# Performance work log

Measured on AMD Instinct MI355X. Metric: run time of the kernel, lower is better.

## Reference

```python
import jax, jax.numpy as jnp
import numpy as np

B, T, D = 4, 2048, 512
E, H, K = 8, 512, 2


def setup_inputs() -> dict:
    key = jax.random.key(0)
    ks = jax.random.split(key, 8)
    s_in = 1.0 / np.sqrt(D)
    s_h = 1.0 / np.sqrt(H)
    return {
        "x": jax.random.normal(ks[0], (B, T, D), dtype=jnp.float32),
        "Wg": jax.random.uniform(ks[1], (D, E), jnp.float32, -s_in, s_in),
        "bg": jax.random.uniform(ks[2], (E,), jnp.float32, -s_in, s_in),
        "W1": jax.random.uniform(ks[3], (E, D, H), jnp.float32, -s_in, s_in),
        "b1": jax.random.uniform(ks[4], (E, H), jnp.float32, -s_in, s_in),
        "W2": jax.random.uniform(ks[5], (E, H, H), jnp.float32, -s_h, s_h),
        "b2": jax.random.uniform(ks[6], (E, H), jnp.float32, -s_h, s_h),
    }


def reference(x, Wg, bg, W1, b1, W2, b2):
    Bx, Tx, Dx = x.shape
    xf = x.reshape(-1, Dx)                                   # [N, D]
    # --- gate (noise_std = 0) ---
    logits = xf @ Wg + bg                                    # [N, E]
    topk_scores, topk_idx = jax.lax.top_k(logits, K)         # [N, K]
    topk_w = jax.nn.softmax(topk_scores, axis=-1)            # K=2 -> softmax over selected
    # --- experts: dense compute, then gather the selected ones ---
    h = jax.nn.gelu(jnp.einsum('nd,edh->neh', xf, W1) + b1, approximate=False)  # [N, E, H]
    y = jnp.einsum('neh,ehf->nef', h, W2) + b2               # [N, E, H]
    sel = jnp.take_along_axis(y, topk_idx[:, :, None], axis=1)  # [N, K, H]
    out = jnp.sum(topk_w[:, :, None] * sel, axis=1)          # weighted combine [N, H]
    return out.reshape(Bx, Tx, -1)
```

## Files before the change

### kernel.cpp

```cpp
#include <hip/hip_runtime.h>
#include <hip/hip_bf16.h>


typedef __bf16 bf16x8 __attribute__((ext_vector_type(8)));
typedef float  f32x4  __attribute__((ext_vector_type(4)));

#define N_TOK 8192
#define D_IN  512
#define N_EXP 8
#define H_DIM 512
#define TILE  32

static __device__ __forceinline__ unsigned short f2bf(float f) {
    union { float f; unsigned u; } v; v.f = f;
    unsigned r = v.u + 0x7FFFu + ((v.u >> 16) & 1u);
    return (unsigned short)(r >> 16);
}
static __device__ __forceinline__ float bf2f(unsigned short h) {
    union { unsigned u; float f; } v; v.u = ((unsigned)h) << 16; return v.f;
}

__global__ void __launch_bounds__(256) k_pack(const float* __restrict__ W1,
                                              const float* __restrict__ W2,
                                              unsigned short* __restrict__ w1f,
                                              unsigned short* __restrict__ w2f) {
    __shared__ float t[32][65];
    int z = blockIdx.z;
    int e = z & 7;
    const float* in = (z < 8) ? W1 : W2;
    unsigned short* out = (z < 8) ? w1f : w2f;
    int cb0 = blockIdx.x * 4;
    int kc  = blockIdx.y;
    const float* src = in + ((size_t)e * 512 + kc * 32) * 512 + blockIdx.x * 64;
    int tid = threadIdx.x;
    int r = tid >> 3, cq = (tid & 7) * 8;
    float4 v0 = *(const float4*)(src + (size_t)r * 512 + cq);
    float4 v1 = *(const float4*)(src + (size_t)r * 512 + cq + 4);
    t[r][cq + 0] = v0.x; t[r][cq + 1] = v0.y; t[r][cq + 2] = v0.z; t[r][cq + 3] = v0.w;
    t[r][cq + 4] = v1.x; t[r][cq + 5] = v1.y; t[r][cq + 6] = v1.z; t[r][cq + 7] = v1.w;
    __syncthreads();
    int g = tid >> 6, lane = tid & 63;
    int l15 = lane & 15, l4 = lane >> 4;
    unsigned v[4];
    #pragma unroll
    for (int j = 0; j < 4; ++j) {
        unsigned lo = f2bf(t[l4 * 8 + 2 * j    ][g * 16 + l15]);
        unsigned hi = f2bf(t[l4 * 8 + 2 * j + 1][g * 16 + l15]);
        v[j] = lo | (hi << 16);
    }
    size_t dst = (((size_t)(e * 32 + cb0 + g) * 16 + kc) * 512) + lane * 8;
    *(uint4*)(out + dst) = make_uint4(v[0], v[1], v[2], v[3]);
}

__global__ void __launch_bounds__(256) k_gate(const float* __restrict__ x,
                                              const float* __restrict__ Wg,
                                              const float* __restrict__ bg,
                                              unsigned char* __restrict__ sel,
                                              float2* __restrict__ w2,
                                              unsigned short* __restrict__ xbf) {
    __shared__ float part[32][8][8];
    __shared__ float lg[32][8];
    int tid = threadIdx.x;
    int t = tid >> 3, c = tid & 7;
    int n0 = blockIdx.x * 32;
    int n = n0 + t;
    const float4* xr = (const float4*)(x + (size_t)n * D_IN + c * 64);
    float acc[8];
    #pragma unroll
    for (int e = 0; e < 8; ++e) acc[e] = 0.f;
    #pragma unroll
    for (int j4 = 0; j4 < 16; ++j4) {
        float4 v = xr[j4];
        int k = c * 64 + j4 * 4;
        float xv[4] = {v.x, v.y, v.z, v.w};
        #pragma unroll
        for (int u = 0; u < 4; ++u) {
            float4 wlo = *(const float4*)(Wg + (size_t)(k + u) * 8);
            float4 whi = *(const float4*)(Wg + (size_t)(k + u) * 8 + 4);
            acc[0] += xv[u] * wlo.x; acc[1] += xv[u] * wlo.y;
            acc[2] += xv[u] * wlo.z; acc[3] += xv[u] * wlo.w;
            acc[4] += xv[u] * whi.x; acc[5] += xv[u] * whi.y;
            acc[6] += xv[u] * whi.z; acc[7] += xv[u] * whi.w;
        }
    }
    #pragma unroll
    for (int e = 0; e < 8; ++e) part[t][c][e] = acc[e];
    __syncthreads();
    {
        float f = bg[c];
        #pragma unroll
        for (int cc = 0; cc < 8; ++cc) f += part[t][cc][c];
        lg[t][c] = f;
    }
    __syncthreads();
    if (c == 0) {
        float best = lg[t][0]; int i1 = 0;
        #pragma unroll
        for (int j = 1; j < 8; ++j) { float v = lg[t][j]; if (v > best) { best = v; i1 = j; } }
        float best2 = -1e30f; int i2 = 0;
        #pragma unroll
        for (int j = 0; j < 8; ++j) {
            if (j == i1) continue;
            float v = lg[t][j]; if (v > best2) { best2 = v; i2 = j; }
        }
        float tt = expf(best2 - best);
        float w0 = 1.0f / (1.0f + tt);
        sel[n] = (unsigned char)(i1 | (i2 << 4));
        w2[n] = make_float2(w0, 1.0f - w0);
    }
    #pragma unroll
    for (int i = 0; i < 8; ++i) {
        int idx = tid + i * 256;
        int r = idx >> 6, g = idx & 63;
        const float* src = x + (size_t)(n0 + r) * D_IN + g * 8;
        float4 a = *(const float4*)src;
        float4 b = *(const float4*)(src + 4);
        unsigned u0 = (unsigned)f2bf(a.x) | ((unsigned)f2bf(a.y) << 16);
        unsigned u1 = (unsigned)f2bf(a.z) | ((unsigned)f2bf(a.w) << 16);
        unsigned u2 = (unsigned)f2bf(b.x) | ((unsigned)f2bf(b.y) << 16);
        unsigned u3 = (unsigned)f2bf(b.z) | ((unsigned)f2bf(b.w) << 16);
        *(uint4*)(xbf + (size_t)(n0 + r) * D_IN + g * 8) = make_uint4(u0, u1, u2, u3);
    }
}

__global__ void __launch_bounds__(1024) k_build(const unsigned char* __restrict__ sel,
                                                const float2* __restrict__ w2,
                                                int* __restrict__ counts,
                                                int* __restrict__ lists,
                                                float* __restrict__ wgts) {
    int e = blockIdx.x;
    __shared__ int wave_tot[16], wave_base[16];
    int tid = threadIdx.x;
    int lane = tid & 63, wv = tid >> 6;
    int base = 0;
    for (int c0 = 0; c0 < N_TOK; c0 += 1024) {
        int n = c0 + tid;
        unsigned char s = sel[n];
        bool f1 = ((s & 15) == e);
        bool f = f1 || ((s >> 4) == e);
        unsigned long long mask = __ballot(f);
        int prefix = __popcll(mask & ((1ull << lane) - 1ull));
        if (lane == 0) wave_tot[wv] = __popcll(mask);
        __syncthreads();
        if (tid < 16) {
            int wb = 0;
            for (int i = 0; i < tid; ++i) wb += wave_tot[i];
            wave_base[tid] = wb;
        }
        __syncthreads();
        if (f) {
            int pos = base + wave_base[wv] + prefix;
            lists[e * N_TOK + pos] = (n << 1) | (f1 ? 0 : 1);
            float2 w = w2[n];
            wgts[e * N_TOK + pos] = f1 ? w.x : w.y;
        }
        base += wave_base[15] + wave_tot[15];
        __syncthreads();
    }
    if (tid == 0) counts[e] = base;
}

template <bool SLOT>
__global__ void __launch_bounds__(512, 4)
k_experts(const unsigned short* __restrict__ xbf,
          const unsigned short* __restrict__ w1f, const float* __restrict__ b1,
          const unsigned short* __restrict__ w2f, const float* __restrict__ b2,
          const int* __restrict__ counts, const int* __restrict__ lists,
          const float* __restrict__ wgts,
          unsigned short* __restrict__ ybuf, float* __restrict__ out) {
    __shared__ unsigned short lds[TILE * D_IN];
    __shared__ int   tl[TILE];
    __shared__ float wl[TILE];

    int b = blockIdx.x;
    int e = b & 7;
    int tile = b >> 3;
    int cnt = counts[e];
    int row0 = tile * TILE;
    if (row0 >= cnt) return;
    int rv = min(TILE, cnt - row0);

    int tid = threadIdx.x;
    int lane = tid & 63;
    int wid = tid >> 6;
    int cw = wid * 64;
    int l15 = lane & 15, l4 = lane >> 4;

    if (tid < TILE) {
        int v = 0; float w = 0.f;
        if (tid < rv) {
            v = lists[e * N_TOK + row0 + tid];
            w = wgts [e * N_TOK + row0 + tid];
        }
        tl[tid] = v; wl[tid] = w;
    }
    __syncthreads();

    #pragma unroll
    for (int it = 0; it < 4; ++it) {
        int idx = tid + it * 512;
        int r = idx >> 6, g = idx & 63;
        uint4 v = make_uint4(0, 0, 0, 0);
        if (r < rv)
            v = *(const uint4*)(xbf + (size_t)(tl[r] >> 1) * D_IN + g * 8);
        int off = (r * 1024 + g * 16) ^ ((r & 7) << 4);
        *(uint4*)((char*)lds + off) = v;
    }
    __syncthreads();

    const unsigned short* w1base = w1f + ((size_t)(e * 32 + wid * 4) * 16) * 512 + (size_t)lane * 8;
    f32x4 acc[2][4];
    #pragma unroll
    for (int n = 0; n < 4; ++n) {
        float bv = b1[e * H_DIM + cw + n * 16 + l15];
        #pragma unroll
        for (int m = 0; m < 2; ++m) acc[m][n] = f32x4{bv, bv, bv, bv};
    }
    {
        bf16x8 bb[4][4];
        #pragma unroll
        for (int n = 0; n < 4; ++n) {
            bb[0][n] = *(const bf16x8*)(w1base + (n * 16 + 0) * 512);
            bb[1][n] = *(const bf16x8*)(w1base + (n * 16 + 1) * 512);
            bb[2][n] = *(const bf16x8*)(w1base + (n * 16 + 2) * 512);
        }
        #pragma unroll
        for (int kc = 0; kc < 16; ++kc) {
            if (kc + 3 < 16) {
                #pragma unroll
                for (int n = 0; n < 4; ++n)
                    bb[(kc + 3) & 3][n] = *(const bf16x8*)(w1base + (n * 16 + kc + 3) * 512);
            }
            int k0 = kc * 32 + l4 * 8;
            bf16x8 a[2];
            #pragma unroll
            for (int m = 0; m < 2; ++m) {
                int row = m * 16 + l15;
                int off = (row * 1024 + k0 * 2) ^ ((row & 7) << 4);
                a[m] = *(const bf16x8*)((const char*)lds + off);
            }
            #pragma unroll
            for (int n = 0; n < 4; ++n)
                #pragma unroll
                for (int m = 0; m < 2; ++m)
                    acc[m][n] = __builtin_amdgcn_mfma_f32_16x16x32_bf16(a[m], bb[kc & 3][n], acc[m][n], 0, 0, 0);
        }
    }
    __syncthreads();

    #pragma unroll
    for (int m = 0; m < 2; ++m)
        #pragma unroll
        for (int n = 0; n < 4; ++n)
            #pragma unroll
            for (int r = 0; r < 4; ++r) {
                int row = m * 16 + l4 * 4 + r;
                int col = cw + n * 16 + l15;
                float v = acc[m][n][r];
                float g = 0.5f * v * (1.0f + erff(v * 0.70710678118654752f));
                int off = (row * 1024 + col * 2) ^ ((row & 7) << 4);
                *(unsigned short*)((char*)lds + off) = f2bf(g);
            }
    __syncthreads();

    const unsigned short* w2base = w2f + ((size_t)(e * 32 + wid * 4) * 16) * 512 + (size_t)lane * 8;
    #pragma unroll
    for (int n = 0; n < 4; ++n) {
        float bv = b2[e * H_DIM + cw + n * 16 + l15];
        #pragma unroll
        for (int m = 0; m < 2; ++m) acc[m][n] = f32x4{bv, bv, bv, bv};
    }
    {
        bf16x8 bb[4][4];
        #pragma unroll
        for (int n = 0; n < 4; ++n) {
            bb[0][n] = *(const bf16x8*)(w2base + (n * 16 + 0) * 512);
            bb[1][n] = *(const bf16x8*)(w2base + (n * 16 + 1) * 512);
            bb[2][n] = *(const bf16x8*)(w2base + (n * 16 + 2) * 512);
        }
        #pragma unroll
        for (int kc = 0; kc < 16; ++kc) {
            if (kc + 3 < 16) {
                #pragma unroll
                for (int n = 0; n < 4; ++n)
                    bb[(kc + 3) & 3][n] = *(const bf16x8*)(w2base + (n * 16 + kc + 3) * 512);
            }
            int k0 = kc * 32 + l4 * 8;
            bf16x8 a[2];
            #pragma unroll
            for (int m = 0; m < 2; ++m) {
                int row = m * 16 + l15;
                int off = (row * 1024 + k0 * 2) ^ ((row & 7) << 4);
                a[m] = *(const bf16x8*)((const char*)lds + off);
            }
            #pragma unroll
            for (int n = 0; n < 4; ++n)
                #pragma unroll
                for (int m = 0; m < 2; ++m)
                    acc[m][n] = __builtin_amdgcn_mfma_f32_16x16x32_bf16(a[m], bb[kc & 3][n], acc[m][n], 0, 0, 0);
        }
    }

    if (SLOT) {
        __syncthreads();
        #pragma unroll
        for (int m = 0; m < 2; ++m)
            #pragma unroll
            for (int n = 0; n < 4; ++n)
                #pragma unroll
                for (int r = 0; r < 4; ++r) {
                    int row = m * 16 + l4 * 4 + r;
                    int col = cw + n * 16 + l15;
                    lds[row * 512 + col] = f2bf(acc[m][n][r] * wl[row]);
                }
        __syncthreads();
        #pragma unroll
        for (int rr = 0; rr < 4; ++rr) {
            int row = wid * 4 + rr;
            if (row < rv) {
                int v = tl[row];
                uint4 d = *(uint4*)((char*)lds + row * 1024 + lane * 16);
                *(uint4*)(ybuf + (size_t)v * H_DIM + lane * 8) = d;
            }
        }
    } else {
        #pragma unroll
        for (int m = 0; m < 2; ++m)
            #pragma unroll
            for (int r = 0; r < 4; ++r) {
                int row = m * 16 + l4 * 4 + r;
                if (row < rv) {
                    int t = tl[row] >> 1;
                    float gw = wl[row];
                    #pragma unroll
                    for (int n = 0; n < 4; ++n) {
                        int col = cw + n * 16 + l15;
                        atomicAdd(out + (size_t)t * H_DIM + col, gw * acc[m][n][r]);
                    }
                }
            }
    }
}

__global__ void __launch_bounds__(256) k_combine(const unsigned short* __restrict__ yb,
                                                 float* __restrict__ out) {
    int gid = blockIdx.x * 256 + threadIdx.x;
    int n = gid >> 6;
    int h0 = (gid & 63) * 8;
    const unsigned short* r0 = yb + ((size_t)2 * n) * H_DIM + h0;
    uint4 a = *(const uint4*)r0;
    uint4 b = *(const uint4*)(r0 + H_DIM);
    float o[8];
    unsigned ua[4] = {a.x, a.y, a.z, a.w}, ub[4] = {b.x, b.y, b.z, b.w};
    #pragma unroll
    for (int j = 0; j < 4; ++j) {
        o[2 * j]     = bf2f((unsigned short)(ua[j] & 0xFFFF)) + bf2f((unsigned short)(ub[j] & 0xFFFF));
        o[2 * j + 1] = bf2f((unsigned short)(ua[j] >> 16))    + bf2f((unsigned short)(ub[j] >> 16));
    }
    float* dst = out + (size_t)n * H_DIM + h0;
    *(float4*)dst       = make_float4(o[0], o[1], o[2], o[3]);
    *(float4*)(dst + 4) = make_float4(o[4], o[5], o[6], o[7]);
}

extern "C" void kernel_launch(void* const* d_in, const int* in_sizes, int n_in,
                              void* d_out, int out_size, void* d_ws, size_t ws_size,
                              hipStream_t stream) {
    (void)in_sizes; (void)n_in;
    const float* x  = (const float*)d_in[0];
    const float* Wg = (const float*)d_in[1];
    const float* bg = (const float*)d_in[2];
    const float* W1 = (const float*)d_in[3];
    const float* b1 = (const float*)d_in[4];
    const float* W2 = (const float*)d_in[5];
    const float* b2 = (const float*)d_in[6];
    float* out = (float*)d_out;

    char* ws = (char*)d_ws;
    unsigned short* w1f = (unsigned short*)(ws);
    unsigned short* w2f = (unsigned short*)(ws + (4u << 20));
    unsigned short* ybuf= (unsigned short*)(ws + (8u << 20));
    unsigned short* xbf = (unsigned short*)(ws + (24u << 20));
    char* tail = ws + (32u << 20);
    int*   counts = (int*)(tail);
    int*   lists  = (int*)(tail + 256);
    float* wgts   = (float*)(tail + 256 + 262144);
    unsigned char* sel = (unsigned char*)(tail + 256 + 524288);
    float2* w2g   = (float2*)(tail + 256 + 532480);
    size_t need = (32u << 20) + 256 + 532480 + 65536;

    bool slot = ws_size >= need;
    if (!slot) {
        xbf  = (unsigned short*)(ws + (8u << 20));
        tail = ws + (16u << 20);
        counts = (int*)(tail);
        lists  = (int*)(tail + 256);
        wgts   = (float*)(tail + 256 + 262144);
        sel    = (unsigned char*)(tail + 256 + 524288);
        w2g    = (float2*)(tail + 256 + 532480);
        hipMemsetAsync(out, 0, (size_t)out_size * sizeof(float), stream);
    }

    k_pack<<<dim3(8, 16, 16), dim3(256), 0, stream>>>(W1, W2, w1f, w2f);
    k_gate<<<dim3(N_TOK / 32), dim3(256), 0, stream>>>(x, Wg, bg, sel, w2g, xbf);
    k_build<<<dim3(N_EXP), dim3(1024), 0, stream>>>(sel, w2g, counts, lists, wgts);
    if (slot) {
        k_experts<true><<<dim3(2048), dim3(512), 0, stream>>>(
            xbf, w1f, b1, w2f, b2, counts, lists, wgts, ybuf, out);
        k_combine<<<dim3(N_TOK * 64 / 256), dim3(256), 0, stream>>>(ybuf, out);
    } else {
        k_experts<false><<<dim3(2048), dim3(512), 0, stream>>>(
            xbf, w1f, b1, w2f, b2, counts, lists, wgts, ybuf, out);
    }
}
```

Before: 191.3 us.

## Double expert row tile to 64 and convert x to bf16 inside expert kernel

Each expert block now processes 64 gathered token rows as two 32-row halves that share every loaded weight fragment. This halves how often W1/W2 are reread from memory and halves the grid size. The separate bf16 copy of x written by the gate kernel is removed; the expert kernel gathers fp32 rows and converts them while staging into LDS. The cost is twice the accumulator registers and LDS per block, lower occupancy (launch bounds 512,2), and more wasted work on partially filled tiles.

```diff
diff --git a/kernel.cpp b/kernel.cpp
--- a/kernel.cpp
+++ b/kernel.cpp
@@ -9,7 +9,7 @@
 #define D_IN  512
 #define N_EXP 8
 #define H_DIM 512
-#define TILE  32
+#define TILE  64
 
 static __device__ __forceinline__ unsigned short f2bf(float f) {
     union { float f; unsigned u; } v; v.f = f;
@@ -56,14 +56,12 @@
                                               const float* __restrict__ Wg,
                                               const float* __restrict__ bg,
                                               unsigned char* __restrict__ sel,
-                                              float2* __restrict__ w2,
-                                              unsigned short* __restrict__ xbf) {
+                                              float2* __restrict__ w2) {
     __shared__ float part[32][8][8];
     __shared__ float lg[32][8];
     int tid = threadIdx.x;
     int t = tid >> 3, c = tid & 7;
-    int n0 = blockIdx.x * 32;
-    int n = n0 + t;
+    int n = blockIdx.x * 32 + t;
     const float4* xr = (const float4*)(x + (size_t)n * D_IN + c * 64);
     float acc[8];
     #pragma unroll
@@ -107,19 +105,6 @@
         float w0 = 1.0f / (1.0f + tt);
         sel[n] = (unsigned char)(i1 | (i2 << 4));
         w2[n] = make_float2(w0, 1.0f - w0);
-    }
-    #pragma unroll
-    for (int i = 0; i < 8; ++i) {
-        int idx = tid + i * 256;
-        int r = idx >> 6, g = idx & 63;
-        const float* src = x + (size_t)(n0 + r) * D_IN + g * 8;
-        float4 a = *(const float4*)src;
-        float4 b = *(const float4*)(src + 4);
-        unsigned u0 = (unsigned)f2bf(a.x) | ((unsigned)f2bf(a.y) << 16);
-        unsigned u1 = (unsigned)f2bf(a.z) | ((unsigned)f2bf(a.w) << 16);
-        unsigned u2 = (unsigned)f2bf(b.x) | ((unsigned)f2bf(b.y) << 16);
-        unsigned u3 = (unsigned)f2bf(b.z) | ((unsigned)f2bf(b.w) << 16);
-        *(uint4*)(xbf + (size_t)(n0 + r) * D_IN + g * 8) = make_uint4(u0, u1, u2, u3);
     }
 }
 
@@ -161,14 +146,15 @@
 }
 
 template <bool SLOT>
-__global__ void __launch_bounds__(512, 4)
-k_experts(const unsigned short* __restrict__ xbf,
+__global__ void __launch_bounds__(512, 2)
+k_experts(const float* __restrict__ x,
           const unsigned short* __restrict__ w1f, const float* __restrict__ b1,
           const unsigned short* __restrict__ w2f, const float* __restrict__ b2,
           const int* __restrict__ counts, const int* __restrict__ lists,
           const float* __restrict__ wgts,
           unsigned short* __restrict__ ybuf, float* __restrict__ out) {
-    __shared__ unsigned short lds[TILE * D_IN];
+    __shared__ unsigned short ldsA[32 * D_IN];
+    __shared__ unsigned short ldsB[32 * D_IN];
     __shared__ int   tl[TILE];
     __shared__ float wl[TILE];
 
@@ -197,53 +183,62 @@
     __syncthreads();
 
     #pragma unroll
-    for (int it = 0; it < 4; ++it) {
+    for (int it = 0; it < 16; ++it) {
         int idx = tid + it * 512;
-        int r = idx >> 6, g = idx & 63;
-        uint4 v = make_uint4(0, 0, 0, 0);
+        int r = idx >> 7, c4 = idx & 127;
+        float4 v = make_float4(0.f, 0.f, 0.f, 0.f);
         if (r < rv)
-            v = *(const uint4*)(xbf + (size_t)(tl[r] >> 1) * D_IN + g * 8);
-        int off = (r * 1024 + g * 16) ^ ((r & 7) << 4);
-        *(uint4*)((char*)lds + off) = v;
-    }
-    __syncthreads();
-
-    const unsigned short* w1base = w1f + ((size_t)(e * 32 + wid * 4) * 16) * 512 + (size_t)lane * 8;
-    f32x4 acc[2][4];
-    #pragma unroll
-    for (int n = 0; n < 4; ++n) {
-        float bv = b1[e * H_DIM + cw + n * 16 + l15];
-        #pragma unroll
-        for (int m = 0; m < 2; ++m) acc[m][n] = f32x4{bv, bv, bv, bv};
-    }
+            v = ((const float4*)(x + (size_t)(tl[r] >> 1) * D_IN))[c4];
+        unsigned lo = (unsigned)f2bf(v.x) | ((unsigned)f2bf(v.y) << 16);
+        unsigned hi = (unsigned)f2bf(v.z) | ((unsigned)f2bf(v.w) << 16);
+        int rr = r & 31;
+        int off = (rr * 1024 + c4 * 8) ^ ((rr & 7) << 4);
+        char* base = (r < 32) ? (char*)ldsA : (char*)ldsB;
+        *(uint2*)(base + off) = make_uint2(lo, hi);
+    }
+    __syncthreads();
+
+    f32x4 accA[2][4], accB[2][4];
+
     {
+        const unsigned short* wbase = w1f + ((size_t)(e * 32 + wid * 4) * 16) * 512 + (size_t)lane * 8;
+        #pragma unroll
+        for (int n = 0; n < 4; ++n) {
+            float bv = b1[e * H_DIM + cw + n * 16 + l15];
+            #pragma unroll
+            for (int m = 0; m < 2; ++m) { accA[m][n] = f32x4{bv, bv, bv, bv}; accB[m][n] = f32x4{bv, bv, bv, bv}; }
+        }
         bf16x8 bb[4][4];
         #pragma unroll
         for (int n = 0; n < 4; ++n) {
-            bb[0][n] = *(const bf16x8*)(w1base + (n * 16 + 0) * 512);
-            bb[1][n] = *(const bf16x8*)(w1base + (n * 16 + 1) * 512);
-            bb[2][n] = *(const bf16x8*)(w1base + (n * 16 + 2) * 512);
+            bb[0][n] = *(const bf16x8*)(wbase + (n * 16 + 0) * 512);
+            bb[1][n] = *(const bf16x8*)(wbase + (n * 16 + 1) * 512);
+            bb[2][n] = *(const bf16x8*)(wbase + (n * 16 + 2) * 512);
         }
         #pragma unroll
         for (int kc = 0; kc < 16; ++kc) {
             if (kc + 3 < 16) {
                 #pragma unroll
                 for (int n = 0; n < 4; ++n)
-                    bb[(kc + 3) & 3][n] = *(const bf16x8*)(w1base + (n * 16 + kc + 3) * 512);
+                    bb[(kc + 3) & 3][n] = *(const bf16x8*)(wbase + (n * 16 + kc + 3) * 512);
             }
             int k0 = kc * 32 + l4 * 8;
-            bf16x8 a[2];
+            bf16x8 aA[2], aB[2];
             #pragma unroll
             for (int m = 0; m < 2; ++m) {
                 int row = m * 16 + l15;
                 int off = (row * 1024 + k0 * 2) ^ ((row & 7) << 4);
-                a[m] = *(const bf16x8*)((const char*)lds + off);
-            }
-            #pragma unroll
-            for (int n = 0; n < 4; ++n)
-                #pragma unroll
-                for (int m = 0; m < 2; ++m)
-                    acc[m][n] = __builtin_amdgcn_mfma_f32_16x16x32_bf16(a[m], bb[kc & 3][n], acc[m][n], 0, 0, 0);
+                aA[m] = *(const bf16x8*)((const char*)ldsA + off);
+                aB[m] = *(const bf16x8*)((const char*)ldsB + off);
+            }
+            #pragma unroll
+            for (int n = 0; n < 4; ++n) {
+                #pragma unroll
+                for (int m = 0; m < 2; ++m) {
+                    accA[m][n] = __builtin_amdgcn_mfma_f32_16x16x32_bf16(aA[m], bb[kc & 3][n], accA[m][n], 0, 0, 0);
+                    accB[m][n] = __builtin_amdgcn_mfma_f32_16x16x32_bf16(aB[m], bb[kc & 3][n], accB[m][n], 0, 0, 0);
+                }
+            }
         }
     }
     __syncthreads();
@@ -256,48 +251,55 @@
             for (int r = 0; r < 4; ++r) {
                 int row = m * 16 + l4 * 4 + r;
                 int col = cw + n * 16 + l15;
-                float v = acc[m][n][r];
-                float g = 0.5f * v * (1.0f + erff(v * 0.70710678118654752f));
                 int off = (row * 1024 + col * 2) ^ ((row & 7) << 4);
-                *(unsigned short*)((char*)lds + off) = f2bf(g);
-            }
-    __syncthreads();
-
-    const unsigned short* w2base = w2f + ((size_t)(e * 32 + wid * 4) * 16) * 512 + (size_t)lane * 8;
-    #pragma unroll
-    for (int n = 0; n < 4; ++n) {
-        float bv = b2[e * H_DIM + cw + n * 16 + l15];
-        #pragma unroll
-        for (int m = 0; m < 2; ++m) acc[m][n] = f32x4{bv, bv, bv, bv};
-    }
+                float vA = accA[m][n][r];
+                float gA = 0.5f * vA * (1.0f + erff(vA * 0.70710678118654752f));
+                *(unsigned short*)((char*)ldsA + off) = f2bf(gA);
+                float vB = accB[m][n][r];
+                float gB = 0.5f * vB * (1.0f + erff(vB * 0.70710678118654752f));
+                *(unsigned short*)((char*)ldsB + off) = f2bf(gB);
+            }
+    __syncthreads();
+
     {
+        const unsigned short* wbase = w2f + ((size_t)(e * 32 + wid * 4) * 16) * 512 + (size_t)lane * 8;
+        #pragma unroll
+        for (int n = 0; n < 4; ++n) {
+            float bv = b2[e * H_DIM + cw + n * 16 + l15];
+            #pragma unroll
+            for (int m = 0; m < 2; ++m) { accA[m][n] = f32x4{bv, bv, bv, bv}; accB[m][n] = f32x4{bv, bv, bv, bv}; }
+        }
         bf16x8 bb[4][4];
         #pragma unroll
         for (int n = 0; n < 4; ++n) {
-            bb[0][n] = *(const bf16x8*)(w2base + (n * 16 + 0) * 512);
-            bb[1][n] = *(const bf16x8*)(w2base + (n * 16 + 1) * 512);
-            bb[2][n] = *(const bf16x8*)(w2base + (n * 16 + 2) * 512);
+            bb[0][n] = *(const bf16x8*)(wbase + (n * 16 + 0) * 512);
+            bb[1][n] = *(const bf16x8*)(wbase + (n * 16 + 1) * 512);
+            bb[2][n] = *(const bf16x8*)(wbase + (n * 16 + 2) * 512);
         }
         #pragma unroll
         for (int kc = 0; kc < 16; ++kc) {
             if (kc + 3 < 16) {
                 #pragma unroll
                 for (int n = 0; n < 4; ++n)
-                    bb[(kc + 3) & 3][n] = *(const bf16x8*)(w2base + (n * 16 + kc + 3) * 512);
+                    bb[(kc + 3) & 3][n] = *(const bf16x8*)(wbase + (n * 16 + kc + 3) * 512);
             }
             int k0 = kc * 32 + l4 * 8;
-            bf16x8 a[2];
+            bf16x8 aA[2], aB[2];
             #pragma unroll
             for (int m = 0; m < 2; ++m) {
                 int row = m * 16 + l15;
                 int off = (row * 1024 + k0 * 2) ^ ((row & 7) << 4);
-                a[m] = *(const bf16x8*)((const char*)lds + off);
-            }
-            #pragma unroll
-            for (int n = 0; n < 4; ++n)
-                #pragma unroll
-                for (int m = 0; m < 2; ++m)
-                    acc[m][n] = __builtin_amdgcn_mfma_f32_16x16x32_bf16(a[m], bb[kc & 3][n], acc[m][n], 0, 0, 0);
+                aA[m] = *(const bf16x8*)((const char*)ldsA + off);
+                aB[m] = *(const bf16x8*)((const char*)ldsB + off);
+            }
+            #pragma unroll
+            for (int n = 0; n < 4; ++n) {
+                #pragma unroll
+                for (int m = 0; m < 2; ++m) {
+                    accA[m][n] = __builtin_amdgcn_mfma_f32_16x16x32_bf16(aA[m], bb[kc & 3][n], accA[m][n], 0, 0, 0);
+                    accB[m][n] = __builtin_amdgcn_mfma_f32_16x16x32_bf16(aB[m], bb[kc & 3][n], accB[m][n], 0, 0, 0);
+                }
+            }
         }
     }
 
@@ -311,15 +313,17 @@
                 for (int r = 0; r < 4; ++r) {
                     int row = m * 16 + l4 * 4 + r;
                     int col = cw + n * 16 + l15;
-                    lds[row * 512 + col] = f2bf(acc[m][n][r] * wl[row]);
+                    ldsA[row * 512 + col] = f2bf(accA[m][n][r] * wl[row]);
+                    ldsB[row * 512 + col] = f2bf(accB[m][n][r] * wl[row + 32]);
                 }
         __syncthreads();
         #pragma unroll
-        for (int rr = 0; rr < 4; ++rr) {
-            int row = wid * 4 + rr;
+        for (int rr = 0; rr < 8; ++rr) {
+            int row = wid * 8 + rr;
             if (row < rv) {
                 int v = tl[row];
-                uint4 d = *(uint4*)((char*)lds + row * 1024 + lane * 16);
+                const unsigned short* src = (row < 32) ? ldsA : ldsB;
+                uint4 d = *(uint4*)((char*)src + (row & 31) * 1024 + lane * 16);
                 *(uint4*)(ybuf + (size_t)v * H_DIM + lane * 8) = d;
             }
         }
@@ -328,15 +332,15 @@
         for (int m = 0; m < 2; ++m)
             #pragma unroll
             for (int r = 0; r < 4; ++r) {
-                int row = m * 16 + l4 * 4 + r;
-                if (row < rv) {
-                    int t = tl[row] >> 1;
-                    float gw = wl[row];
-                    #pragma unroll
-                    for (int n = 0; n < 4; ++n) {
-                        int col = cw + n * 16 + l15;
-                        atomicAdd(out + (size_t)t * H_DIM + col, gw * acc[m][n][r]);
-                    }
+                int rowA = m * 16 + l4 * 4 + r;
+                int rowB = rowA + 32;
+                #pragma unroll
+                for (int n = 0; n < 4; ++n) {
+                    int col = cw + n * 16 + l15;
+                    if (rowA < rv)
+                        atomicAdd(out + (size_t)(tl[rowA] >> 1) * H_DIM + col, wl[rowA] * accA[m][n][r]);
+                    if (rowB < rv)
+                        atomicAdd(out + (size_t)(tl[rowB] >> 1) * H_DIM + col, wl[rowB] * accB[m][n][r]);
                 }
             }
     }
@@ -379,19 +383,17 @@
     unsigned short* w1f = (unsigned short*)(ws);
     unsigned short* w2f = (unsigned short*)(ws + (4u << 20));
     unsigned short* ybuf= (unsigned short*)(ws + (8u << 20));
-    unsigned short* xbf = (unsigned short*)(ws + (24u << 20));
-    char* tail = ws + (32u << 20);
+    char* tail = ws + (24u << 20);
     int*   counts = (int*)(tail);
     int*   lists  = (int*)(tail + 256);
     float* wgts   = (float*)(tail + 256 + 262144);
     unsigned char* sel = (unsigned char*)(tail + 256 + 524288);
     float2* w2g   = (float2*)(tail + 256 + 532480);
-    size_t need = (32u << 20) + 256 + 532480 + 65536;
+    size_t need = (24u << 20) + 256 + 532480 + 65536;
 
     bool slot = ws_size >= need;
     if (!slot) {
-        xbf  = (unsigned short*)(ws + (8u << 20));
-        tail = ws + (16u << 20);
+        tail = ws + (8u << 20);
         counts = (int*)(tail);
         lists  = (int*)(tail + 256);
         wgts   = (float*)(tail + 256 + 262144);
@@ -401,14 +403,14 @@
     }
 
     k_pack<<<dim3(8, 16, 16), dim3(256), 0, stream>>>(W1, W2, w1f, w2f);
-    k_gate<<<dim3(N_TOK / 32), dim3(256), 0, stream>>>(x, Wg, bg, sel, w2g, xbf);
+    k_gate<<<dim3(N_TOK / 32), dim3(256), 0, stream>>>(x, Wg, bg, sel, w2g);
     k_build<<<dim3(N_EXP), dim3(1024), 0, stream>>>(sel, w2g, counts, lists, wgts);
     if (slot) {
-        k_experts<true><<<dim3(2048), dim3(512), 0, stream>>>(
-            xbf, w1f, b1, w2f, b2, counts, lists, wgts, ybuf, out);
+        k_experts<true><<<dim3(1024), dim3(512), 0, stream>>>(
+            x, w1f, b1, w2f, b2, counts, lists, wgts, ybuf, out);
         k_combine<<<dim3(N_TOK * 64 / 256), dim3(256), 0, stream>>>(ybuf, out);
     } else {
-        k_experts<false><<<dim3(2048), dim3(512), 0, stream>>>(
-            xbf, w1f, b1, w2f, b2, counts, lists, wgts, ybuf, out);
-    }
-}
+        k_experts<false><<<dim3(1024), dim3(512), 0, stream>>>(
+            x, w1f, b1, w2f, b2, counts, lists, wgts, ybuf, out);
+    }
+}
```

Result: no change. 188.1 us (-1.7%).

## Split fused expert MLP into separate layer kernels with 64-row tiles

Applied to the files above, without the earlier changes.

The single fused expert kernel (32-row tiles, both layers in one block) becomes two kernels. k_l1 gathers fp32 x rows, converts them to bf16 in LDS, and writes GELU(h) as bf16 to a padded global buffer. k_l2 reads that buffer and applies the second layer. Each block now handles 64 rows and half of the output columns, so every weight fragment is reused across more rows, and the x-to-bf16 conversion in the gate kernel is removed. The cost is an extra global write and read of the hidden activations, an additional launch, and 64KB of LDS per block, which may limit occupancy.

```diff
diff --git a/kernel.cpp b/kernel.cpp
--- a/kernel.cpp
+++ b/kernel.cpp
@@ -9,7 +9,6 @@
 #define D_IN  512
 #define N_EXP 8
 #define H_DIM 512
-#define TILE  32
 
 static __device__ __forceinline__ unsigned short f2bf(float f) {
     union { float f; unsigned u; } v; v.f = f;
@@ -18,6 +17,9 @@
 }
 static __device__ __forceinline__ float bf2f(unsigned short h) {
     union { unsigned u; float f; } v; v.u = ((unsigned)h) << 16; return v.f;
+}
+static __device__ __forceinline__ float gelu_exact(float v) {
+    return 0.5f * v * (1.0f + erff(v * 0.70710678118654752f));
 }
 
 __global__ void __launch_bounds__(256) k_pack(const float* __restrict__ W1,
@@ -56,14 +58,12 @@
                                               const float* __restrict__ Wg,
                                               const float* __restrict__ bg,
                                               unsigned char* __restrict__ sel,
-                                              float2* __restrict__ w2,
-                                              unsigned short* __restrict__ xbf) {
+                                              float2* __restrict__ w2) {
     __shared__ float part[32][8][8];
     __shared__ float lg[32][8];
     int tid = threadIdx.x;
     int t = tid >> 3, c = tid & 7;
-    int n0 = blockIdx.x * 32;
-    int n = n0 + t;
+    int n = blockIdx.x * 32 + t;
     const float4* xr = (const float4*)(x + (size_t)n * D_IN + c * 64);
     float acc[8];
     #pragma unroll
@@ -107,19 +107,6 @@
         float w0 = 1.0f / (1.0f + tt);
         sel[n] = (unsigned char)(i1 | (i2 << 4));
         w2[n] = make_float2(w0, 1.0f - w0);
-    }
-    #pragma unroll
-    for (int i = 0; i < 8; ++i) {
-        int idx = tid + i * 256;
-        int r = idx >> 6, g = idx & 63;
-        const float* src = x + (size_t)(n0 + r) * D_IN + g * 8;
-        float4 a = *(const float4*)src;
-        float4 b = *(const float4*)(src + 4);
-        unsigned u0 = (unsigned)f2bf(a.x) | ((unsigned)f2bf(a.y) << 16);
-        unsigned u1 = (unsigned)f2bf(a.z) | ((unsigned)f2bf(a.w) << 16);
-        unsigned u2 = (unsigned)f2bf(b.x) | ((unsigned)f2bf(b.y) << 16);
-        unsigned u3 = (unsigned)f2bf(b.z) | ((unsigned)f2bf(b.w) << 16);
-        *(uint4*)(xbf + (size_t)(n0 + r) * D_IN + g * 8) = make_uint4(u0, u1, u2, u3);
     }
 }
 
@@ -160,33 +147,132 @@
     if (tid == 0) counts[e] = base;
 }
 
+__global__ void __launch_bounds__(512, 4)
+k_l1(const float* __restrict__ x,
+     const unsigned short* __restrict__ w1f, const float* __restrict__ b1,
+     const int* __restrict__ counts, const int* __restrict__ lists,
+     unsigned short* __restrict__ hbuf) {
+    __shared__ unsigned short lds[64 * D_IN];
+    __shared__ int tl[64];
+
+    int b = blockIdx.x;
+    int e = b & 7;
+    int rest = b >> 3;
+    int tile = rest >> 1, ch = rest & 1;
+    int cnt = counts[e];
+    int row0 = tile * 64;
+    if (row0 >= cnt) return;
+    int rv = min(64, cnt - row0);
+    int gb = row0;
+    #pragma unroll
+    for (int i = 0; i < 8; ++i) gb += (i < e) ? ((counts[i] + 63) & ~63) : 0;
+
+    int tid = threadIdx.x, lane = tid & 63, wid = tid >> 6;
+    int l15 = lane & 15, l4 = lane >> 4;
+    if (tid < 64) tl[tid] = (tid < rv) ? lists[e * N_TOK + row0 + tid] : 0;
+
+    const unsigned short* wbase = w1f + ((size_t)(e * 32 + ch * 16 + wid * 2) * 16) * 512 + (size_t)lane * 8;
+    bf16x8 bb[3][2];
+    #pragma unroll
+    for (int n = 0; n < 2; ++n) {
+        bb[0][n] = *(const bf16x8*)(wbase + (n * 16 + 0) * 512);
+        bb[1][n] = *(const bf16x8*)(wbase + (n * 16 + 1) * 512);
+    }
+    float bv[2];
+    #pragma unroll
+    for (int n = 0; n < 2; ++n) bv[n] = b1[e * H_DIM + ch * 256 + wid * 32 + n * 16 + l15];
+    __syncthreads();
+
+    #pragma unroll
+    for (int it = 0; it < 16; ++it) {
+        int idx = tid + it * 512;
+        int r = idx >> 7, c4 = idx & 127;
+        float4 v = make_float4(0.f, 0.f, 0.f, 0.f);
+        if (r < rv)
+            v = ((const float4*)(x + (size_t)(tl[r] >> 1) * D_IN))[c4];
+        unsigned lo = (unsigned)f2bf(v.x) | ((unsigned)f2bf(v.y) << 16);
+        unsigned hi = (unsigned)f2bf(v.z) | ((unsigned)f2bf(v.w) << 16);
+        int off = (r * 1024 + c4 * 8) ^ ((r & 7) << 4);
+        *(uint2*)((char*)lds + off) = make_uint2(lo, hi);
+    }
+    __syncthreads();
+
+    f32x4 acc[4][2];
+    #pragma unroll
+    for (int n = 0; n < 2; ++n)
+        #pragma unroll
+        for (int m = 0; m < 4; ++m) acc[m][n] = f32x4{bv[n], bv[n], bv[n], bv[n]};
+
+    #pragma unroll
+    for (int kc = 0; kc < 16; ++kc) {
+        if (kc + 2 < 16) {
+            #pragma unroll
+            for (int n = 0; n < 2; ++n)
+                bb[(kc + 2) % 3][n] = *(const bf16x8*)(wbase + (n * 16 + kc + 2) * 512);
+        }
+        int k0 = kc * 32 + l4 * 8;
+        bf16x8 a[4];
+        #pragma unroll
+        for (int m = 0; m < 4; ++m) {
+            int row = m * 16 + l15;
+            int off = (row * 1024 + k0 * 2) ^ ((row & 7) << 4);
+            a[m] = *(const bf16x8*)((const char*)lds + off);
+        }
+        #pragma unroll
+        for (int n = 0; n < 2; ++n)
+            #pragma unroll
+            for (int m = 0; m < 4; ++m)
+                acc[m][n] = __builtin_amdgcn_mfma_f32_16x16x32_bf16(a[m], bb[kc % 3][n], acc[m][n], 0, 0, 0);
+    }
+    __syncthreads();
+
+    #pragma unroll
+    for (int m = 0; m < 4; ++m)
+        #pragma unroll
+        for (int n = 0; n < 2; ++n)
+            #pragma unroll
+            for (int r = 0; r < 4; ++r) {
+                int row = m * 16 + l4 * 4 + r;
+                int lcol = wid * 32 + n * 16 + l15;
+                lds[row * 256 + lcol] = f2bf(gelu_exact(acc[m][n][r]));
+            }
+    __syncthreads();
+    #pragma unroll
+    for (int it = 0; it < 4; ++it) {
+        int idx = tid + it * 512;
+        int row = idx >> 5, g = idx & 31;
+        if (row < rv)
+            *(uint4*)(hbuf + (size_t)(gb + row) * 512 + ch * 256 + g * 8) =
+                *(uint4*)(lds + row * 256 + g * 8);
+    }
+}
+
 template <bool SLOT>
 __global__ void __launch_bounds__(512, 4)
-k_experts(const unsigned short* __restrict__ xbf,
-          const unsigned short* __restrict__ w1f, const float* __restrict__ b1,
-          const unsigned short* __restrict__ w2f, const float* __restrict__ b2,
-          const int* __restrict__ counts, const int* __restrict__ lists,
-          const float* __restrict__ wgts,
-          unsigned short* __restrict__ ybuf, float* __restrict__ out) {
-    __shared__ unsigned short lds[TILE * D_IN];
-    __shared__ int   tl[TILE];
-    __shared__ float wl[TILE];
+k_l2(const unsigned short* __restrict__ hbuf,
+     const unsigned short* __restrict__ w2f, const float* __restrict__ b2,
+     const int* __restrict__ counts, const int* __restrict__ lists,
+     const float* __restrict__ wgts,
+     unsigned short* __restrict__ ybuf, float* __restrict__ out) {
+    __shared__ unsigned short lds[64 * D_IN];
+    __shared__ int   tl[64];
+    __shared__ float wl[64];
 
     int b = blockIdx.x;
     int e = b & 7;
-    int tile = b >> 3;
+    int rest = b >> 3;
+    int tile = rest >> 1, ch = rest & 1;
     int cnt = counts[e];
-    int row0 = tile * TILE;
+    int row0 = tile * 64;
     if (row0 >= cnt) return;
-    int rv = min(TILE, cnt - row0);
-
-    int tid = threadIdx.x;
-    int lane = tid & 63;
-    int wid = tid >> 6;
-    int cw = wid * 64;
+    int rv = min(64, cnt - row0);
+    int gb = row0;
+    #pragma unroll
+    for (int i = 0; i < 8; ++i) gb += (i < e) ? ((counts[i] + 63) & ~63) : 0;
+
+    int tid = threadIdx.x, lane = tid & 63, wid = tid >> 6;
     int l15 = lane & 15, l4 = lane >> 4;
-
-    if (tid < TILE) {
+    if (tid < 64) {
         int v = 0; float w = 0.f;
         if (tid < rv) {
             v = lists[e * N_TOK + row0 + tid];
@@ -194,138 +280,83 @@
         }
         tl[tid] = v; wl[tid] = w;
     }
-    __syncthreads();
-
-    #pragma unroll
-    for (int it = 0; it < 4; ++it) {
+
+    const unsigned short* wbase = w2f + ((size_t)(e * 32 + ch * 16 + wid * 2) * 16) * 512 + (size_t)lane * 8;
+    bf16x8 bb[3][2];
+    #pragma unroll
+    for (int n = 0; n < 2; ++n) {
+        bb[0][n] = *(const bf16x8*)(wbase + (n * 16 + 0) * 512);
+        bb[1][n] = *(const bf16x8*)(wbase + (n * 16 + 1) * 512);
+    }
+    float bv[2];
+    #pragma unroll
+    for (int n = 0; n < 2; ++n) bv[n] = b2[e * H_DIM + ch * 256 + wid * 32 + n * 16 + l15];
+    __syncthreads();
+
+    #pragma unroll
+    for (int it = 0; it < 8; ++it) {
         int idx = tid + it * 512;
         int r = idx >> 6, g = idx & 63;
         uint4 v = make_uint4(0, 0, 0, 0);
         if (r < rv)
-            v = *(const uint4*)(xbf + (size_t)(tl[r] >> 1) * D_IN + g * 8);
+            v = *(const uint4*)(hbuf + (size_t)(gb + r) * 512 + g * 8);
         int off = (r * 1024 + g * 16) ^ ((r & 7) << 4);
         *(uint4*)((char*)lds + off) = v;
     }
     __syncthreads();
 
-    const unsigned short* w1base = w1f + ((size_t)(e * 32 + wid * 4) * 16) * 512 + (size_t)lane * 8;
-    f32x4 acc[2][4];
-    #pragma unroll
-    for (int n = 0; n < 4; ++n) {
-        float bv = b1[e * H_DIM + cw + n * 16 + l15];
-        #pragma unroll
-        for (int m = 0; m < 2; ++m) acc[m][n] = f32x4{bv, bv, bv, bv};
-    }
-    {
-        bf16x8 bb[4][4];
-        #pragma unroll
-        for (int n = 0; n < 4; ++n) {
-            bb[0][n] = *(const bf16x8*)(w1base + (n * 16 + 0) * 512);
-            bb[1][n] = *(const bf16x8*)(w1base + (n * 16 + 1) * 512);
-            bb[2][n] = *(const bf16x8*)(w1base + (n * 16 + 2) * 512);
-        }
-        #pragma unroll
-        for (int kc = 0; kc < 16; ++kc) {
-            if (kc + 3 < 16) {
-                #pragma unroll
-                for (int n = 0; n < 4; ++n)
-                    bb[(kc + 3) & 3][n] = *(const bf16x8*)(w1base + (n * 16 + kc + 3) * 512);
-            }
-            int k0 = kc * 32 + l4 * 8;
-            bf16x8 a[2];
-            #pragma unroll
-            for (int m = 0; m < 2; ++m) {
-                int row = m * 16 + l15;
-                int off = (row * 1024 + k0 * 2) ^ ((row & 7) << 4);
-                a[m] = *(const bf16x8*)((const char*)lds + off);
-            }
-            #pragma unroll
-            for (int n = 0; n < 4; ++n)
-                #pragma unroll
-                for (int m = 0; m < 2; ++m)
-                    acc[m][n] = __builtin_amdgcn_mfma_f32_16x16x32_bf16(a[m], bb[kc & 3][n], acc[m][n], 0, 0, 0);
-        }
-    }
-    __syncthreads();
-
-    #pragma unroll
-    for (int m = 0; m < 2; ++m)
-        #pragma unroll
-        for (int n = 0; n < 4; ++n)
-            #pragma unroll
-            for (int r = 0; r < 4; ++r) {
-                int row = m * 16 + l4 * 4 + r;
-                int col = cw + n * 16 + l15;
-                float v = acc[m][n][r];
-                float g = 0.5f * v * (1.0f + erff(v * 0.70710678118654752f));
-                int off = (row * 1024 + col * 2) ^ ((row & 7) << 4);
-                *(unsigned short*)((char*)lds + off) = f2bf(g);
-            }
-    __syncthreads();
-
-    const unsigned short* w2base = w2f + ((size_t)(e * 32 + wid * 4) * 16) * 512 + (size_t)lane * 8;
-    #pragma unroll
-    for (int n = 0; n < 4; ++n) {
-        float bv = b2[e * H_DIM + cw + n * 16 + l15];
-        #pragma unroll
-        for (int m = 0; m < 2; ++m) acc[m][n] = f32x4{bv, bv, bv, bv};
-    }
-    {
-        bf16x8 bb[4][4];
-        #pragma unroll
-        for (int n = 0; n < 4; ++n) {
-            bb[0][n] = *(const bf16x8*)(w2base + (n * 16 + 0) * 512);
-            bb[1][n] = *(const bf16x8*)(w2base + (n * 16 + 1) * 512);
-            bb[2][n] = *(const bf16x8*)(w2base + (n * 16 + 2) * 512);
-        }
-        #pragma unroll
-        for (int kc = 0; kc < 16; ++kc) {
-            if (kc + 3 < 16) {
-                #pragma unroll
-                for (int n = 0; n < 4; ++n)
-                    bb[(kc + 3) & 3][n] = *(const bf16x8*)(w2base + (n * 16 + kc + 3) * 512);
-            }
-            int k0 = kc * 32 + l4 * 8;
-            bf16x8 a[2];
-            #pragma unroll
-            for (int m = 0; m < 2; ++m) {
-                int row = m * 16 + l15;
-                int off = (row * 1024 + k0 * 2) ^ ((row & 7) << 4);
-                a[m] = *(const bf16x8*)((const char*)lds + off);
-            }
-            #pragma unroll
-            for (int n = 0; n < 4; ++n)
-                #pragma unroll
-                for (int m = 0; m < 2; ++m)
-                    acc[m][n] = __builtin_amdgcn_mfma_f32_16x16x32_bf16(a[m], bb[kc & 3][n], acc[m][n], 0, 0, 0);
-        }
+    f32x4 acc[4][2];
+    #pragma unroll
+    for (int n = 0; n < 2; ++n)
+        #pragma unroll
+        for (int m = 0; m < 4; ++m) acc[m][n] = f32x4{bv[n], bv[n], bv[n], bv[n]};
+
+    #pragma unroll
+    for (int kc = 0; kc < 16; ++kc) {
+        if (kc + 2 < 16) {
+            #pragma unroll
+            for (int n = 0; n < 2; ++n)
+                bb[(kc + 2) % 3][n] = *(const bf16x8*)(wbase + (n * 16 + kc + 2) * 512);
+        }
+        int k0 = kc * 32 + l4 * 8;
+        bf16x8 a[4];
+        #pragma unroll
+        for (int m = 0; m < 4; ++m) {
+            int row = m * 16 + l15;
+            int off = (row * 1024 + k0 * 2) ^ ((row & 7) << 4);
+            a[m] = *(const bf16x8*)((const char*)lds + off);
+        }
+        #pragma unroll
+        for (int n = 0; n < 2; ++n)
+            #pragma unroll
+            for (int m = 0; m < 4; ++m)
+                acc[m][n] = __builtin_amdgcn_mfma_f32_16x16x32_bf16(a[m], bb[kc % 3][n], acc[m][n], 0, 0, 0);
     }
 
     if (SLOT) {
         __syncthreads();
         #pragma unroll
-        for (int m = 0; m < 2; ++m)
-            #pragma unroll
-            for (int n = 0; n < 4; ++n)
+        for (int m = 0; m < 4; ++m)
+            #pragma unroll
+            for (int n = 0; n < 2; ++n)
                 #pragma unroll
                 for (int r = 0; r < 4; ++r) {
                     int row = m * 16 + l4 * 4 + r;
-                    int col = cw + n * 16 + l15;
-                    lds[row * 512 + col] = f2bf(acc[m][n][r] * wl[row]);
+                    int lcol = wid * 32 + n * 16 + l15;
+                    lds[row * 256 + lcol] = f2bf(acc[m][n][r] * wl[row]);
                 }
         __syncthreads();
         #pragma unroll
-        for (int rr = 0; rr < 4; ++rr) {
-            int row = wid * 4 + rr;
-            if (row < rv) {
-                int v = tl[row];
-                uint4 d = *(uint4*)((char*)lds + row * 1024 + lane * 16);
-                *(uint4*)(ybuf + (size_t)v * H_DIM + lane * 8) = d;
-            }
+        for (int it = 0; it < 4; ++it) {
+            int idx = tid + it * 512;
+            int row = idx >> 5, g = idx & 31;
+            if (row < rv)
+                *(uint4*)(ybuf + (size_t)tl[row] * 512 + ch * 256 + g * 8) =
+                    *(uint4*)(lds + row * 256 + g * 8);
         }
     } else {
         #pragma unroll
-        for (int m = 0; m < 2; ++m)
+        for (int m = 0; m < 4; ++m)
             #pragma unroll
             for (int r = 0; r < 4; ++r) {
                 int row = m * 16 + l4 * 4 + r;
@@ -333,8 +364,8 @@
                     int t = tl[row] >> 1;
                     float gw = wl[row];
                     #pragma unroll
-                    for (int n = 0; n < 4; ++n) {
-                        int col = cw + n * 16 + l15;
+                    for (int n = 0; n < 2; ++n) {
+                        int col = ch * 256 + wid * 32 + n * 16 + l15;
                         atomicAdd(out + (size_t)t * H_DIM + col, gw * acc[m][n][r]);
                     }
                 }
@@ -376,39 +407,49 @@
     float* out = (float*)d_out;
 
     char* ws = (char*)d_ws;
+    const size_t tail_sz = 256 + 262144 + 262144 + 8192 + 65536;
+    size_t need1 = (41ull << 20) + tail_sz;
+    size_t need2 = (25ull << 20) + tail_sz;
+
     unsigned short* w1f = (unsigned short*)(ws);
-    unsigned short* w2f = (unsigned short*)(ws + (4u << 20));
-    unsigned short* ybuf= (unsigned short*)(ws + (8u << 20));
-    unsigned short* xbf = (unsigned short*)(ws + (24u << 20));
-    char* tail = ws + (32u << 20);
+    unsigned short* w2f = (unsigned short*)(ws + (4ull << 20));
+    unsigned short* ybuf = nullptr;
+    unsigned short* hbuf = nullptr;
+    char* tail;
+    int mode;
+    if (ws_size >= need1) {
+        mode = 0;
+        ybuf = (unsigned short*)(ws + (8ull << 20));
+        hbuf = (unsigned short*)(ws + (24ull << 20));
+        tail = ws + (41ull << 20);
+    } else if (ws_size >= need2) {
+        mode = 1;
+        hbuf = (unsigned short*)(ws + (8ull << 20));
+        tail = ws + (25ull << 20);
+    } else {
+        mode = 1;
+        hbuf = (unsigned short*)(ws + (8ull << 20));
+        tail = ws + (25ull << 20);
+    }
     int*   counts = (int*)(tail);
     int*   lists  = (int*)(tail + 256);
     float* wgts   = (float*)(tail + 256 + 262144);
     unsigned char* sel = (unsigned char*)(tail + 256 + 524288);
     float2* w2g   = (float2*)(tail + 256 + 532480);
-    size_t need = (32u << 20) + 256 + 532480 + 65536;
-
-    bool slot = ws_size >= need;
-    if (!slot) {
-        xbf  = (unsigned short*)(ws + (8u << 20));
-        tail = ws + (16u << 20);
-        counts = (int*)(tail);
-        lists  = (int*)(tail + 256);
-        wgts   = (float*)(tail + 256 + 262144);
-        sel    = (unsigned char*)(tail + 256 + 524288);
-        w2g    = (float2*)(tail + 256 + 532480);
+
+    if (mode == 1)
         hipMemsetAsync(out, 0, (size_t)out_size * sizeof(float), stream);
-    }
 
     k_pack<<<dim3(8, 16, 16), dim3(256), 0, stream>>>(W1, W2, w1f, w2f);
-    k_gate<<<dim3(N_TOK / 32), dim3(256), 0, stream>>>(x, Wg, bg, sel, w2g, xbf);
+    k_gate<<<dim3(N_TOK / 32), dim3(256), 0, stream>>>(x, Wg, bg, sel, w2g);
     k_build<<<dim3(N_EXP), dim3(1024), 0, stream>>>(sel, w2g, counts, lists, wgts);
-    if (slot) {
-        k_experts<true><<<dim3(2048), dim3(512), 0, stream>>>(
-            xbf, w1f, b1, w2f, b2, counts, lists, wgts, ybuf, out);
+    k_l1<<<dim3(2048), dim3(512), 0, stream>>>(x, w1f, b1, counts, lists, hbuf);
+    if (mode == 0) {
+        k_l2<true><<<dim3(2048), dim3(512), 0, stream>>>(
+            hbuf, w2f, b2, counts, lists, wgts, ybuf, out);
         k_combine<<<dim3(N_TOK * 64 / 256), dim3(256), 0, stream>>>(ybuf, out);
     } else {
-        k_experts<false><<<dim3(2048), dim3(512), 0, stream>>>(
-            xbf, w1f, b1, w2f, b2, counts, lists, wgts, ybuf, out);
-    }
-}
+        k_l2<false><<<dim3(2048), dim3(512), 0, stream>>>(
+            hbuf, w2f, b2, counts, lists, wgts, hbuf , out);
+    }
+}
```

Result: faster. 175.3 us (-8.4%).
